# Performance work log

Measured on AMD Instinct MI355X. Metric: run time of the kernel, lower is better.

## Reference

```python
import jax, jax.numpy as jnp
import numpy as np
import math

B, L, D = 4, 2048, 768
N_HEADS = 12
CHUNK = 8  # query_mask=1 every CHUNK tokens -> f = B*L/CHUNK, f % B == 0
VOCAB = 50000


def setup_inputs() -> dict:
    key = jax.random.key(0)
    ks = jax.random.split(key, 8)
    scale = 1.0 / math.sqrt(D)
    x_qk = jax.random.normal(ks[0], (B, L, D), jnp.float32)
    x_v = jax.random.normal(ks[1], (B, L, D), jnp.float32)
    # deterministic query mask: feature boundary every CHUNK tokens
    pos = jnp.arange(L)
    query_mask = jnp.tile((pos % CHUNK == 0).astype(jnp.int32)[None, :], (B, 1))
    input_ids = jax.random.randint(ks[2], (B, L), 2, VOCAB).astype(jnp.int64)
    # make the last 16 tokens of each row padding to exercise the pad mask
    input_ids = input_ids.at[:, -16:].set(1)
    Wq = jax.random.normal(ks[3], (D, D), jnp.float32) * scale
    Wk = jax.random.normal(ks[4], (D, D), jnp.float32) * scale
    Wv = jax.random.normal(ks[5], (D, D), jnp.float32) * scale
    Wo = jax.random.normal(ks[6], (D, D), jnp.float32) * scale
    zb = jnp.zeros((D,), jnp.float32)
    return {"x_qk": x_qk, "x_v": x_v, "query_mask": query_mask,
            "input_ids": input_ids, "pad_token_id": 1,
            "Wq": Wq, "bq": zb, "Wk": Wk, "bk": zb,
            "Wv": Wv, "bv": zb, "Wo": Wo, "bo": zb}


def reference(x_qk, x_v, query_mask, input_ids, pad_token_id,
              Wq, bq, Wk, bk, Wv, bv, Wo, bo):
    b, l, d = x_qk.shape
    n = b * l
    qm = query_mask.reshape(-1)
    f = int(np.asarray(jnp.sum(qm)))  # static feature count (f % b == 0)
    idx = jnp.nonzero(qm == 1, size=f)[0]                     # [f] query positions
    # segment boundaries: [left_i, right_i) per feature
    left = idx
    right = jnp.concatenate([idx[1:], jnp.array([n], idx.dtype)])
    pos = jnp.arange(n)
    seg_mask = (pos[None, :] >= left[:, None]) & (pos[None, :] < right[:, None])
    seg_mask = seg_mask & (input_ids.reshape(-1) != pad_token_id)[None, :]  # [f, n]

    xq = x_qk.reshape(n, d)
    xv = x_v.reshape(n, d)
    query = xq[idx]                                           # [f, d]
    q = query @ Wq.T + bq                                     # [f, d]
    k = xq @ Wk.T + bk                                        # [n, d]
    v = xv @ Wv.T + bv                                        # [n, d]

    dh = d // N_HEADS
    qh = q.reshape(f, N_HEADS, dh).transpose(1, 0, 2)         # [h, f, dh]
    kh = k.reshape(n, N_HEADS, dh).transpose(1, 0, 2)         # [h, n, dh]
    vh = v.reshape(n, N_HEADS, dh).transpose(1, 0, 2)         # [h, n, dh]

    bias = (1.0 - seg_mask.astype(jnp.float32)) * -10000.0    # [f, n]
    scores = jnp.einsum('hfd,hnd->hfn', qh, kh) / math.sqrt(dh) + bias[None]
    attn = jax.nn.softmax(scores, axis=-1)                    # [h, f, n]
    out = jnp.einsum('hfn,hnd->hfd', attn, vh)                # [h, f, dh]
    out = out.transpose(1, 0, 2).reshape(f, d)
    out = out @ Wo.T + bo
    return out.reshape(b, f // b, d)
```

## Files before the change

### kernel.cpp

```cpp
#include <hip/hip_runtime.h>

#define DMODEL 768
#define NHEADS 12
#define MAXFULL 16
#define NSTEP 24

typedef __attribute__((ext_vector_type(8))) short short8;
typedef __attribute__((ext_vector_type(4))) float f32x4;

__device__ __forceinline__ unsigned pack2_bf16(float a, float b) {
  unsigned ua = __float_as_uint(a), ub = __float_as_uint(b);
  ua = (ua + 0x7fffu + ((ua >> 16) & 1u)) >> 16;
  ub = (ub + 0x7fffu + ((ub >> 16) & 1u)) & 0xffff0000u;
  return ua | ub;
}
__device__ __forceinline__ unsigned short bf16_1(float a) {
  unsigned ua = __float_as_uint(a);
  return (unsigned short)((ua + 0x7fffu + ((ua >> 16) & 1u)) >> 16);
}

__device__ __forceinline__ void load16_lds(const void* g, void* l) {
  __builtin_amdgcn_global_load_lds(
      (const __attribute__((address_space(1))) unsigned int*)g,
      (__attribute__((address_space(3))) unsigned int*)l, 16, 0, 0);
}

__global__ __launch_bounds__(256) void convW(const float* __restrict__ w0,
    const float* __restrict__ w1, const float* __restrict__ w2,
    const float* __restrict__ w3, unsigned* __restrict__ o0,
    unsigned* __restrict__ o1, unsigned* __restrict__ o2,
    unsigned* __restrict__ o3, int count) {
  const int nv = count >> 2;
  const float* src[4] = {w0, w1, w2, w3};
  unsigned* dst[4] = {o0, o1, o2, o3};
  for (int idx = blockIdx.x * 256 + threadIdx.x; idx < 4 * nv;
       idx += gridDim.x * 256) {
    int m = idx / nv, r = idx - m * nv;
    float4 v = ((const float4*)src[m])[r];
    dst[m][2 * r]     = pack2_bf16(v.x, v.y);
    dst[m][2 * r + 1] = pack2_bf16(v.z, v.w);
  }
}

__global__ __launch_bounds__(256) void convX(const float* __restrict__ x0,
    const float* __restrict__ x1, unsigned* __restrict__ o0,
    unsigned* __restrict__ o1, int count) {
  const int nv = count >> 2;
  for (int idx = blockIdx.x * 256 + threadIdx.x; idx < 2 * nv;
       idx += gridDim.x * 256) {
    int m = idx / nv, r = idx - m * nv;
    float4 v = m ? ((const float4*)x1)[r] : ((const float4*)x0)[r];
    unsigned* d = m ? o1 : o0;
    d[2 * r]     = pack2_bf16(v.x, v.y);
    d[2 * r + 1] = pack2_bf16(v.z, v.w);
  }
}

struct GSeg {
  const unsigned short* A;
  const unsigned short* W;
  const float* bias;
  const int* row_map;
  float* C;
  int base;
};

__device__ __forceinline__ void stage_step(const GSeg& d, int k0, int arow0,
    int arow1, int wrow0, int wrow1, int skc, unsigned short* AsB,
    unsigned short* BsB, int woff) {
  load16_lds(d.A + (size_t)arow0 * DMODEL + k0 + skc, AsB + woff);
  load16_lds(d.A + (size_t)arow1 * DMODEL + k0 + skc, AsB + woff + 16 * 32);
  load16_lds(d.W + (size_t)wrow0 * DMODEL + k0 + skc, BsB + woff);
  load16_lds(d.W + (size_t)wrow1 * DMODEL + k0 + skc, BsB + woff + 16 * 32);
}

__device__ __forceinline__ void compute_step(const unsigned short* AsB,
    const unsigned short* BsB, int wm, int wn, int m16, int quad,
    f32x4 acc[4][4]) {
  short8 a[4], b[4];
#pragma unroll
  for (int i = 0; i < 4; ++i)
    a[i] = *(const short8*)&AsB[(wm + i * 16 + m16) * 32 + quad * 8];
#pragma unroll
  for (int j2 = 0; j2 < 4; ++j2)
    b[j2] = *(const short8*)&BsB[(wn + j2 * 16 + m16) * 32 + quad * 8];
#pragma unroll
  for (int i = 0; i < 4; ++i)
#pragma unroll
    for (int j2 = 0; j2 < 4; ++j2)
      acc[i][j2] = __builtin_amdgcn_mfma_f32_16x16x32_bf16(a[i], b[j2], acc[i][j2], 0, 0, 0);
}

__global__ __launch_bounds__(256) void gemm128(GSeg g0, GSeg g1, GSeg g2) {
  __shared__ __attribute__((aligned(16))) unsigned short As[3][128 * 32];
  __shared__ __attribute__((aligned(16))) unsigned short Bs[3][128 * 32];
  const int t = threadIdx.x;
  const int id = blockIdx.x;
  const GSeg& d = (id >= g2.base) ? g2 : ((id >= g1.base) ? g1 : g0);
  const int lid = id - d.base;
  const int xcd = lid & 7, j = lid >> 3;
  const int bn = (j % 6) * 128;
  const int bm = ((j / 6) * 8 + xcd) * 128;
  const int lane = t & 63, wid = t >> 6;
  const int m16 = lane & 15, quad = lane >> 4;
  const int wm = (wid >> 1) * 64, wn = (wid & 1) * 64;

  f32x4 acc[4][4];
#pragma unroll
  for (int i = 0; i < 4; ++i)
#pragma unroll
    for (int j2 = 0; j2 < 4; ++j2) acc[i][j2] = (f32x4){0.f, 0.f, 0.f, 0.f};

  const int srow = wid * 32 + (lane >> 2);
  const int skc = (lane & 3) * 8;
  int arow0, arow1;
  if (d.row_map) {
    arow0 = d.row_map[bm + srow];
    arow1 = d.row_map[bm + srow + 16];
  } else {
    arow0 = bm + srow;
    arow1 = bm + srow + 16;
  }
  const int wrow0 = bn + srow, wrow1 = bn + srow + 16;
  const int woff = (wid * 32) * 32;

  stage_step(d, 0,  arow0, arow1, wrow0, wrow1, skc, &As[0][0], &Bs[0][0], woff);
  stage_step(d, 32, arow0, arow1, wrow0, wrow1, skc, &As[1][0], &Bs[1][0], woff);
  stage_step(d, 64, arow0, arow1, wrow0, wrow1, skc, &As[2][0], &Bs[2][0], woff);

#pragma unroll 1
  for (int g = 0; g < (NSTEP - 3) / 3; ++g) {
    const int t0 = g * 3;
#pragma unroll
    for (int u = 0; u < 3; ++u) {
      const int ts = t0 + u;
      asm volatile("s_waitcnt vmcnt(8)" ::: "memory");
      __builtin_amdgcn_s_barrier();
      __builtin_amdgcn_sched_barrier(0);
      compute_step(&As[u][0], &Bs[u][0], wm, wn, m16, quad, acc);
      __builtin_amdgcn_s_barrier();
      __builtin_amdgcn_sched_barrier(0);
      stage_step(d, (ts + 3) * 32, arow0, arow1, wrow0, wrow1, skc,
                 &As[u][0], &Bs[u][0], woff);
    }
  }
  asm volatile("s_waitcnt vmcnt(8)" ::: "memory");
  __builtin_amdgcn_s_barrier();
  __builtin_amdgcn_sched_barrier(0);
  compute_step(&As[0][0], &Bs[0][0], wm, wn, m16, quad, acc);
  asm volatile("s_waitcnt vmcnt(4)" ::: "memory");
  __builtin_amdgcn_s_barrier();
  __builtin_amdgcn_sched_barrier(0);
  compute_step(&As[1][0], &Bs[1][0], wm, wn, m16, quad, acc);
  asm volatile("s_waitcnt vmcnt(0)" ::: "memory");
  __builtin_amdgcn_s_barrier();
  __builtin_amdgcn_sched_barrier(0);
  compute_step(&As[2][0], &Bs[2][0], wm, wn, m16, quad, acc);

  float bv[4]; int bcol[4];
#pragma unroll
  for (int j2 = 0; j2 < 4; ++j2) {
    bcol[j2] = bn + wn + j2 * 16 + m16;
    bv[j2] = d.bias[bcol[j2]];
  }
#pragma unroll
  for (int i = 0; i < 4; ++i) {
    const int rbase = bm + wm + i * 16 + quad * 4;
#pragma unroll
    for (int r = 0; r < 4; ++r) {
      const int row = rbase + r;
#pragma unroll
      for (int j2 = 0; j2 < 4; ++j2)
        d.C[(size_t)row * DMODEL + bcol[j2]] = acc[i][j2][r] + bv[j2];
    }
  }
}

__global__ __launch_bounds__(1024) void build_segments(const int* __restrict__ qm,
    const int* __restrict__ ids, const int* __restrict__ padp,
    int n, int f, int* __restrict__ left, int* __restrict__ right,
    int* __restrict__ nvalid, int* __restrict__ fullrank,
    int* __restrict__ fullist, int* __restrict__ nfull) {
  __shared__ int cnt[1024];
  __shared__ int fullcnt;
  const int t = threadIdx.x;
  if (t == 0) fullcnt = 0;
  const int per = (n + 1023) >> 10;
  const int base = t * per;
  int c = 0;
  for (int i = 0; i < per; ++i) {
    int p = base + i;
    if (p < n && qm[p] != 0) ++c;
  }
  cnt[t] = c;
  __syncthreads();
  for (int off = 1; off < 1024; off <<= 1) {
    int v = (t >= off) ? cnt[t - off] : 0;
    __syncthreads();
    cnt[t] += v;
    __syncthreads();
  }
  int r = cnt[t] - c;
  for (int i = 0; i < per; ++i) {
    int p = base + i;
    if (p < n && qm[p] != 0) {
      if (r < f) left[r] = p;
      ++r;
    }
  }
  __syncthreads();
  const int pad = *padp;
  for (int i = t; i < f; i += 1024) {
    int L0 = left[i];
    int R0 = (i + 1 < f) ? left[i + 1] : n;
    right[i] = R0;
    int cv = 0;
    for (int p = L0; p < R0; ++p) cv += (ids[p] != pad) ? 1 : 0;
    nvalid[i] = cv;
    if (cv == 0) {
      int rk = atomicAdd(&fullcnt, 1);
      if (rk < MAXFULL) { fullist[rk] = i; fullrank[i] = rk; }
      else fullrank[i] = -1;
    } else {
      fullrank[i] = -1;
    }
  }
  __syncthreads();
  if (t == 0) *nfull = (fullcnt < MAXFULL) ? fullcnt : MAXFULL;
}

__device__ __forceinline__ float allreduce64(float x) {
#pragma unroll
  for (int m = 1; m < 64; m <<= 1) x += __shfl_xor(x, m, 64);
  return x;
}

__global__ __launch_bounds__(256) void attn_seg(const float* __restrict__ q,
    const float* __restrict__ k, const float* __restrict__ v,
    const int* __restrict__ left, const int* __restrict__ right,
    const int* __restrict__ nvalid, const int* __restrict__ ids,
    const int* __restrict__ padp, unsigned short* __restrict__ out) {
  const int wid = threadIdx.x >> 6, lane = threadIdx.x & 63;
  const int feat = blockIdx.x * 4 + wid, h = blockIdx.y;
  if (nvalid[feat] == 0) return;
  const int off = h * 64 + lane;
  const int pad = *padp;
  const float qv = q[(size_t)feat * DMODEL + off];
  float m = -1e30f, l = 0.f, acc = 0.f;
  const int L0 = left[feat], R0 = right[feat];
  for (int p = L0; p < R0; ++p) {
    if (ids[p] == pad) continue;
    float s = allreduce64(qv * k[(size_t)p * DMODEL + off]) * 0.125f;
    float mn = fmaxf(m, s);
    float al = __expf(m - mn);
    float w = __expf(s - mn);
    l = l * al + w;
    acc = acc * al + w * v[(size_t)p * DMODEL + off];
    m = mn;
  }
  out[(size_t)feat * DMODEL + off] = bf16_1(acc / l);
}

__global__ __launch_bounds__(256) void attn_full_part(const float* __restrict__ q,
    const float* __restrict__ k, const float* __restrict__ v,
    const int* __restrict__ fullist, const int* __restrict__ nfullp,
    int n, int P, float* __restrict__ pm, float* __restrict__ pl,
    float* __restrict__ pacc) {
  const int nfull = *nfullp;
  if (nfull == 0) return;
  const int t = threadIdx.x, lane = t & 63, wv = t >> 6;
  const int gw = blockIdx.x * 4 + wv;
  const int h = gw / P, piece = gw - h * P;
  const int pk = n / P;

  __shared__ float q_lds[8 * 64];
  __shared__ float w_lds[4][64 * 8];

  for (int idx = t; idx < 8 * 64; idx += 256) {
    int fl = idx >> 6, d = idx & 63;
    q_lds[idx] = (fl < nfull) ? q[(size_t)fullist[fl] * DMODEL + h * 64 + d] : 0.f;
  }
  __syncthreads();

  float m[8], l[8], acc[8];
#pragma unroll
  for (int f_ = 0; f_ < 8; ++f_) { m[f_] = -1e30f; l[f_] = 0.f; acc[f_] = 0.f; }

  for (int c = 0; c < pk; c += 64) {
    const int pc = piece * pk + c;
    float s[8];
#pragma unroll
    for (int f_ = 0; f_ < 8; ++f_) s[f_] = 0.f;
    const float4* kp = (const float4*)(k + (size_t)(pc + lane) * DMODEL + h * 64);
#pragma unroll 1
    for (int g = 0; g < 2; ++g) {
      float4 kv0 = kp[g * 8 + 0], kv1 = kp[g * 8 + 1], kv2 = kp[g * 8 + 2],
             kv3 = kp[g * 8 + 3], kv4 = kp[g * 8 + 4], kv5 = kp[g * 8 + 5],
             kv6 = kp[g * 8 + 6], kv7 = kp[g * 8 + 7];
      const float4* qb = (const float4*)&q_lds[g * 32];
#pragma unroll
      for (int f_ = 0; f_ < 8; ++f_) {
        float4 q0 = qb[f_ * 16 + 0], q1 = qb[f_ * 16 + 1], q2 = qb[f_ * 16 + 2],
               q3 = qb[f_ * 16 + 3], q4 = qb[f_ * 16 + 4], q5 = qb[f_ * 16 + 5],
               q6 = qb[f_ * 16 + 6], q7 = qb[f_ * 16 + 7];
        float acc0 = q0.x * kv0.x + q0.y * kv0.y + q0.z * kv0.z + q0.w * kv0.w;
        acc0 += q1.x * kv1.x + q1.y * kv1.y + q1.z * kv1.z + q1.w * kv1.w;
        acc0 += q2.x * kv2.x + q2.y * kv2.y + q2.z * kv2.z + q2.w * kv2.w;
        acc0 += q3.x * kv3.x + q3.y * kv3.y + q3.z * kv3.z + q3.w * kv3.w;
        acc0 += q4.x * kv4.x + q4.y * kv4.y + q4.z * kv4.z + q4.w * kv4.w;
        acc0 += q5.x * kv5.x + q5.y * kv5.y + q5.z * kv5.z + q5.w * kv5.w;
        acc0 += q6.x * kv6.x + q6.y * kv6.y + q6.z * kv6.z + q6.w * kv6.w;
        acc0 += q7.x * kv7.x + q7.y * kv7.y + q7.z * kv7.z + q7.w * kv7.w;
        s[f_] += acc0;
      }
    }
    float mx[8];
#pragma unroll
    for (int f_ = 0; f_ < 8; ++f_) mx[f_] = s[f_] * 0.125f;
#pragma unroll
    for (int f_ = 0; f_ < 8; ++f_) s[f_] = mx[f_];
#pragma unroll
    for (int st = 1; st < 64; st <<= 1)
#pragma unroll
      for (int f_ = 0; f_ < 8; ++f_) mx[f_] = fmaxf(mx[f_], __shfl_xor(mx[f_], st, 64));
    float alpha[8], w[8], sum[8];
#pragma unroll
    for (int f_ = 0; f_ < 8; ++f_) {
      float mn = fmaxf(m[f_], mx[f_]);
      alpha[f_] = __expf(m[f_] - mn);
      w[f_] = __expf(s[f_] - mn);
      m[f_] = mn;
      sum[f_] = w[f_];
    }
#pragma unroll
    for (int st = 1; st < 64; st <<= 1)
#pragma unroll
      for (int f_ = 0; f_ < 8; ++f_) sum[f_] += __shfl_xor(sum[f_], st, 64);
#pragma unroll
    for (int f_ = 0; f_ < 8; ++f_) l[f_] = l[f_] * alpha[f_] + sum[f_];
    *(float4*)&w_lds[wv][lane * 8]     = make_float4(w[0], w[1], w[2], w[3]);
    *(float4*)&w_lds[wv][lane * 8 + 4] = make_float4(w[4], w[5], w[6], w[7]);
#pragma unroll
    for (int f_ = 0; f_ < 8; ++f_) acc[f_] *= alpha[f_];
    const float* vb = v + (size_t)pc * DMODEL + h * 64 + lane;
#pragma unroll 4
    for (int kk = 0; kk < 64; ++kk) {
      float vd = vb[(size_t)kk * DMODEL];
      float4 wa = *(const float4*)&w_lds[wv][kk * 8];
      float4 wb = *(const float4*)&w_lds[wv][kk * 8 + 4];
      acc[0] += wa.x * vd; acc[1] += wa.y * vd; acc[2] += wa.z * vd; acc[3] += wa.w * vd;
      acc[4] += wb.x * vd; acc[5] += wb.y * vd; acc[6] += wb.z * vd; acc[7] += wb.w * vd;
    }
  }

  for (int f_ = 0; f_ < nfull; ++f_) {
    size_t idx = ((size_t)f_ * NHEADS + h) * P + piece;
    if (lane == 0) { pm[idx] = m[f_]; pl[idx] = l[f_]; }
    pacc[idx * 64 + lane] = acc[f_];
  }
}

__global__ __launch_bounds__(256) void attn_full_comb(
    const int* __restrict__ fullist, const int* __restrict__ nfullp,
    int P, const float* __restrict__ pm, const float* __restrict__ pl,
    const float* __restrict__ pacc, unsigned short* __restrict__ out) {
  const int fl = blockIdx.x, h = blockIdx.y;
  if (fl >= *nfullp) return;
  const int feat = fullist[fl];
  const int t = threadIdx.x, lane = t & 63, wv = t >> 6;
  const size_t base = ((size_t)fl * NHEADS + h) * P;

  __shared__ float s_pm[128];
  __shared__ float s_sc[128];
  __shared__ float s_red[4];
  __shared__ float s_part[4][64];

  for (int sp = t; sp < P; sp += 256) s_pm[sp] = pm[base + sp];
  __syncthreads();
  float mloc = -1e30f;
  for (int sp = t; sp < P; sp += 256) mloc = fmaxf(mloc, s_pm[sp]);
#pragma unroll
  for (int st = 1; st < 64; st <<= 1) mloc = fmaxf(mloc, __shfl_xor(mloc, st, 64));
  if (lane == 0) s_red[wv] = mloc;
  __syncthreads();
  const float M = fmaxf(fmaxf(s_red[0], s_red[1]), fmaxf(s_red[2], s_red[3]));
  __syncthreads();
  float lloc = 0.f;
  for (int sp = t; sp < P; sp += 256) {
    float sc = __expf(s_pm[sp] - M);
    s_sc[sp] = sc;
    lloc += pl[base + sp] * sc;
  }
#pragma unroll
  for (int st = 1; st < 64; st <<= 1) lloc += __shfl_xor(lloc, st, 64);
  if (lane == 0) s_red[wv] = lloc;
  __syncthreads();
  const float Lt = s_red[0] + s_red[1] + s_red[2] + s_red[3];
  float At = 0.f;
  for (int sp = wv; sp < P; sp += 4)
    At += pacc[(base + sp) * 64 + lane] * s_sc[sp];
  s_part[wv][lane] = At;
  __syncthreads();
  if (wv == 0) {
    float tot = s_part[0][lane] + s_part[1][lane] + s_part[2][lane] + s_part[3][lane];
    out[(size_t)feat * DMODEL + h * 64 + lane] = bf16_1(tot / Lt);
  }
}

extern "C" void kernel_launch(void* const* d_in, const int* in_sizes, int n_in,
                              void* d_out, int out_size, void* d_ws, size_t ws_size,
                              hipStream_t stream) {
  const float* x_qk = (const float*)d_in[0];
  const float* x_v  = (const float*)d_in[1];
  const int* qm     = (const int*)d_in[2];
  const int* ids    = (const int*)d_in[3];
  const int* padp   = (const int*)d_in[4];
  const float* Wq = (const float*)d_in[5];
  const float* bq = (const float*)d_in[6];
  const float* Wk = (const float*)d_in[7];
  const float* bk = (const float*)d_in[8];
  const float* Wv = (const float*)d_in[9];
  const float* bv = (const float*)d_in[10];
  const float* Wo = (const float*)d_in[11];
  const float* bo = (const float*)d_in[12];

  const int n = in_sizes[0] / DMODEL;
  const int f = out_size / DMODEL;

  float* kf = (float*)d_ws;
  float* vf = kf + (size_t)n * DMODEL;
  float* qf = vf + (size_t)n * DMODEL;
  unsigned short* af = (unsigned short*)(qf + (size_t)f * DMODEL);
  unsigned short* wqb = af + (size_t)f * DMODEL;
  unsigned short* wkb = wqb + DMODEL * DMODEL;
  unsigned short* wvb = wkb + DMODEL * DMODEL;
  unsigned short* wob = wvb + DMODEL * DMODEL;
  unsigned short* xqb = wob + DMODEL * DMODEL;
  unsigned short* xvb = xqb + (size_t)n * DMODEL;
  int* left     = (int*)(xvb + (size_t)n * DMODEL);
  int* right    = left + f;
  int* nvalid   = right + f;
  int* fullrank = nvalid + f;
  int* fullist  = fullrank + f;
  int* nfull    = fullist + MAXFULL;
  size_t off_bytes = ((size_t)((char*)(nfull + 1) - (char*)d_ws) + 255) & ~(size_t)255;
  int P = 128;
  while (P > 16) {
    size_t need = (size_t)MAXFULL * NHEADS * P * 66 * sizeof(float);
    if (off_bytes + need <= ws_size && (n / P) % 64 == 0 && n % P == 0) break;
    P >>= 1;
  }
  float* pm = (float*)((char*)d_ws + off_bytes);
  float* pl = pm + (size_t)MAXFULL * NHEADS * P;
  float* pacc = pl + (size_t)MAXFULL * NHEADS * P;

  build_segments<<<1, 1024, 0, stream>>>(qm, ids, padp, n, f, left, right,
                                         nvalid, fullrank, fullist, nfull);
  convW<<<1152, 256, 0, stream>>>(Wq, Wk, Wv, Wo, (unsigned*)wqb, (unsigned*)wkb,
                                  (unsigned*)wvb, (unsigned*)wob, DMODEL * DMODEL);
  convX<<<2048, 256, 0, stream>>>(x_qk, x_v, (unsigned*)xqb, (unsigned*)xvb,
                                  n * DMODEL);

  const int TKV = 6 * (n / 128);
  const int TF  = 6 * (f / 128);
  GSeg g0 = { xqb, wkb, bk, nullptr, kf, 0 };
  GSeg g1 = { xvb, wvb, bv, nullptr, vf, TKV };
  GSeg g2 = { xqb, wqb, bq, left,    qf, 2 * TKV };
  gemm128<<<2 * TKV + TF, 256, 0, stream>>>(g0, g1, g2);

  attn_seg<<<dim3(f / 4, NHEADS), 256, 0, stream>>>(qf, kf, vf, left, right,
                                                    nvalid, ids, padp, af);
  attn_full_part<<<NHEADS * P / 4, 256, 0, stream>>>(qf, kf, vf, fullist, nfull,
                                                     n, P, pm, pl, pacc);
  attn_full_comb<<<dim3(MAXFULL, NHEADS), 256, 0, stream>>>(fullist, nfull, P,
                                                            pm, pl, pacc, af);

  GSeg gout = { af, wob, bo, nullptr, (float*)d_out, 0 };
  GSeg gnull = { af, wob, bo, nullptr, (float*)d_out, 1 << 30 };
  gemm128<<<TF, 256, 0, stream>>>(gout, gnull, gnull);
}
```

Baseline: 232.3 us.

## Swizzle GEMM LDS layout, raise MFMA priority, specialize 8-token attention segments

The GEMM now applies an XOR swizzle to the k-chunk column, both when staging tiles into LDS and when reading fragments, so that ds_read bank conflicts are reduced. It also raises wave priority around the MFMA block. The segment attention kernel runs one wave per block and gains a fast path for 8-token segments: all K/V loads are issued together and the eight dot-product reductions are interleaved, which avoids a serial online softmax with dependent shuffles. Correctness relies on the staging swizzle and the read swizzle agreeing per row, and 64-thread blocks may reduce occupancy efficiency.

```diff
diff --git a/kernel.cpp b/kernel.cpp
--- a/kernel.cpp
+++ b/kernel.cpp
@@ -75,20 +75,22 @@
 }
 
 __device__ __forceinline__ void compute_step(const unsigned short* AsB,
-    const unsigned short* BsB, int wm, int wn, int m16, int quad,
+    const unsigned short* BsB, int wm, int wn, int m16, int qx,
     f32x4 acc[4][4]) {
   short8 a[4], b[4];
 #pragma unroll
   for (int i = 0; i < 4; ++i)
-    a[i] = *(const short8*)&AsB[(wm + i * 16 + m16) * 32 + quad * 8];
+    a[i] = *(const short8*)&AsB[(wm + i * 16 + m16) * 32 + qx * 8];
 #pragma unroll
   for (int j2 = 0; j2 < 4; ++j2)
-    b[j2] = *(const short8*)&BsB[(wn + j2 * 16 + m16) * 32 + quad * 8];
+    b[j2] = *(const short8*)&BsB[(wn + j2 * 16 + m16) * 32 + qx * 8];
+  __builtin_amdgcn_s_setprio(1);
 #pragma unroll
   for (int i = 0; i < 4; ++i)
 #pragma unroll
     for (int j2 = 0; j2 < 4; ++j2)
       acc[i][j2] = __builtin_amdgcn_mfma_f32_16x16x32_bf16(a[i], b[j2], acc[i][j2], 0, 0, 0);
+  __builtin_amdgcn_s_setprio(0);
 }
 
 __global__ __launch_bounds__(256) void gemm128(GSeg g0, GSeg g1, GSeg g2) {
@@ -103,6 +105,7 @@
   const int bm = ((j / 6) * 8 + xcd) * 128;
   const int lane = t & 63, wid = t >> 6;
   const int m16 = lane & 15, quad = lane >> 4;
+  const int qx = quad ^ ((m16 >> 1) & 3);
   const int wm = (wid >> 1) * 64, wn = (wid & 1) * 64;
 
   f32x4 acc[4][4];
@@ -112,7 +115,7 @@
     for (int j2 = 0; j2 < 4; ++j2) acc[i][j2] = (f32x4){0.f, 0.f, 0.f, 0.f};
 
   const int srow = wid * 32 + (lane >> 2);
-  const int skc = (lane & 3) * 8;
+  const int skc = ((lane & 3) ^ ((lane >> 3) & 3)) * 8;
   int arow0, arow1;
   if (d.row_map) {
     arow0 = d.row_map[bm + srow];
@@ -137,7 +140,7 @@
       asm volatile("s_waitcnt vmcnt(8)" ::: "memory");
       __builtin_amdgcn_s_barrier();
       __builtin_amdgcn_sched_barrier(0);
-      compute_step(&As[u][0], &Bs[u][0], wm, wn, m16, quad, acc);
+      compute_step(&As[u][0], &Bs[u][0], wm, wn, m16, qx, acc);
       __builtin_amdgcn_s_barrier();
       __builtin_amdgcn_sched_barrier(0);
       stage_step(d, (ts + 3) * 32, arow0, arow1, wrow0, wrow1, skc,
@@ -147,15 +150,15 @@
   asm volatile("s_waitcnt vmcnt(8)" ::: "memory");
   __builtin_amdgcn_s_barrier();
   __builtin_amdgcn_sched_barrier(0);
-  compute_step(&As[0][0], &Bs[0][0], wm, wn, m16, quad, acc);
+  compute_step(&As[0][0], &Bs[0][0], wm, wn, m16, qx, acc);
   asm volatile("s_waitcnt vmcnt(4)" ::: "memory");
   __builtin_amdgcn_s_barrier();
   __builtin_amdgcn_sched_barrier(0);
-  compute_step(&As[1][0], &Bs[1][0], wm, wn, m16, quad, acc);
+  compute_step(&As[1][0], &Bs[1][0], wm, wn, m16, qx, acc);
   asm volatile("s_waitcnt vmcnt(0)" ::: "memory");
   __builtin_amdgcn_s_barrier();
   __builtin_amdgcn_sched_barrier(0);
-  compute_step(&As[2][0], &Bs[2][0], wm, wn, m16, quad, acc);
+  compute_step(&As[2][0], &Bs[2][0], wm, wn, m16, qx, acc);
 
   float bv[4]; int bcol[4];
 #pragma unroll
@@ -235,19 +238,49 @@
   return x;
 }
 
-__global__ __launch_bounds__(256) void attn_seg(const float* __restrict__ q,
+__global__ __launch_bounds__(64) void attn_seg(const float* __restrict__ q,
     const float* __restrict__ k, const float* __restrict__ v,
     const int* __restrict__ left, const int* __restrict__ right,
     const int* __restrict__ nvalid, const int* __restrict__ ids,
     const int* __restrict__ padp, unsigned short* __restrict__ out) {
-  const int wid = threadIdx.x >> 6, lane = threadIdx.x & 63;
-  const int feat = blockIdx.x * 4 + wid, h = blockIdx.y;
+  const int feat = blockIdx.x, h = blockIdx.y, lane = threadIdx.x;
   if (nvalid[feat] == 0) return;
   const int off = h * 64 + lane;
   const int pad = *padp;
   const float qv = q[(size_t)feat * DMODEL + off];
+  const int L0 = left[feat], R0 = right[feat];
+  if (R0 - L0 == 8) {
+    float kv[8], vv[8], s[8];
+    int live[8];
+#pragma unroll
+    for (int p = 0; p < 8; ++p) {
+      kv[p] = k[(size_t)(L0 + p) * DMODEL + off];
+      vv[p] = v[(size_t)(L0 + p) * DMODEL + off];
+      live[p] = (ids[L0 + p] != pad);
+    }
+#pragma unroll
+    for (int p = 0; p < 8; ++p) s[p] = qv * kv[p];
+#pragma unroll
+    for (int m_ = 1; m_ < 64; m_ <<= 1)
+#pragma unroll
+      for (int p = 0; p < 8; ++p) s[p] += __shfl_xor(s[p], m_, 64);
+    float mx = -1e30f;
+#pragma unroll
+    for (int p = 0; p < 8; ++p) {
+      s[p] = live[p] ? s[p] * 0.125f : -1e30f;
+      mx = fmaxf(mx, s[p]);
+    }
+    float l = 0.f, acc = 0.f;
+#pragma unroll
+    for (int p = 0; p < 8; ++p) {
+      float w = __expf(s[p] - mx);
+      l += w;
+      acc += w * vv[p];
+    }
+    out[(size_t)feat * DMODEL + off] = bf16_1(acc / l);
+    return;
+  }
   float m = -1e30f, l = 0.f, acc = 0.f;
-  const int L0 = left[feat], R0 = right[feat];
   for (int p = L0; p < R0; ++p) {
     if (ids[p] == pad) continue;
     float s = allreduce64(qv * k[(size_t)p * DMODEL + off]) * 0.125f;
@@ -468,8 +501,8 @@
   GSeg g2 = { xqb, wqb, bq, left,    qf, 2 * TKV };
   gemm128<<<2 * TKV + TF, 256, 0, stream>>>(g0, g1, g2);
 
-  attn_seg<<<dim3(f / 4, NHEADS), 256, 0, stream>>>(qf, kf, vf, left, right,
-                                                    nvalid, ids, padp, af);
+  attn_seg<<<dim3(f, NHEADS), 64, 0, stream>>>(qf, kf, vf, left, right, nvalid,
+                                               ids, padp, af);
   attn_full_part<<<NHEADS * P / 4, 256, 0, stream>>>(qf, kf, vf, fullist, nfull,
                                                      n, P, pm, pl, pacc);
   attn_full_comb<<<dim3(MAXFULL, NHEADS), 256, 0, stream>>>(fullist, nfull, P,
```

After: 228.2 us. Within noise of the previous version (-1.8%).
